# Kernel tuning notes

Hardware: AMD Instinct MI355X
Metric: run time of the kernel (lower is better)

The kernel has to match this reference:

```python
import jax, jax.numpy as jnp
import numpy as np

B, C, Q = 16, 1024, 128
XD, YD = 64, 32
D, H, HID, L = 512, 8, 2048, 6
HD = D // H
NEG = -1e9


def setup_inputs() -> dict:
    key = jax.random.key(0)
    ks = jax.random.split(key, 12)
    rn = lambda k, shape, s: jax.random.normal(k, shape, jnp.float32) * s
    return {
        "x_c": rn(ks[0], (B, C, XD), 1.0),
        "y_c": rn(ks[1], (B, C, YD), 1.0),
        "x_q": rn(ks[2], (B, Q, XD), 1.0),
        "W_val": rn(ks[3], (XD + YD, D), (XD + YD) ** -0.5),
        "b_val": jnp.zeros((D,), jnp.float32),
        "q_emb": rn(ks[4], (D,), D ** -0.5),
        "in_proj_w": rn(ks[5], (L, 3 * D, D), D ** -0.5),
        "in_proj_b": jnp.zeros((L, 3 * D), jnp.float32),
        "out_w": rn(ks[6], (L, D, D), D ** -0.5),
        "out_b": jnp.zeros((L, D), jnp.float32),
        "ln1_g": jnp.ones((L, D), jnp.float32),
        "ln1_b": jnp.zeros((L, D), jnp.float32),
        "lin1_w": rn(ks[7], (L, HID, D), D ** -0.5),
        "lin1_b": jnp.zeros((L, HID), jnp.float32),
        "lin2_w": rn(ks[8], (L, D, HID), HID ** -0.5),
        "lin2_b": jnp.zeros((L, D), jnp.float32),
        "ln2_g": jnp.ones((L, D), jnp.float32),
        "ln2_b": jnp.zeros((L, D), jnp.float32),
        "W_head": rn(ks[9], (D, YD), D ** -0.5),
        "b_head": jnp.zeros((YD,), jnp.float32),
    }


def _layernorm(x, g, b):
    mu = x.mean(-1, keepdims=True)
    var = ((x - mu) ** 2).mean(-1, keepdims=True)
    return (x - mu) * jax.lax.rsqrt(var + 1e-5) * g + b


def _forward(x_c, y_c, x_q, W_val, b_val, q_emb, in_proj_w, in_proj_b, out_w,
             out_b, ln1_g, ln1_b, lin1_w, lin1_b, lin2_w, lin2_b, ln2_g, ln2_b,
             W_head, b_head):
    bsz, c_len, _ = x_c.shape
    q_len = x_q.shape[1]
    S = c_len + q_len
    # concat y onto x; queries get zero y placeholder
    xy_c = jnp.concatenate([x_c, y_c], axis=-1)
    xy_q = jnp.concatenate([x_q, jnp.zeros((bsz, q_len, y_c.shape[-1]), x_q.dtype)], axis=-1)
    xy = jnp.concatenate([xy_c, xy_q], axis=1) @ W_val + b_val          # [B,S,D]
    xy = xy.at[:, -q_len:].add(q_emb)
    # src_mask: no one may attend to query positions (last q_len keys)
    bias = jnp.where(jnp.arange(S) >= c_len, jnp.float32(NEG), jnp.float32(0.0))  # [S] key axis

    def layer(x, p):
        ipw, ipb, ow, ob, g1, b1, w1, bb1, w2, bb2, g2, b2 = p
        qkv = x @ ipw.T + ipb                                           # [B,S,3D]
        q, k, v = jnp.split(qkv, 3, axis=-1)
        heads = lambda t: t.reshape(bsz, S, H, HD).transpose(0, 2, 1, 3)  # [B,H,S,HD]
        q, k, v = heads(q), heads(k), heads(v)
        scores = jnp.einsum('bhqd,bhkd->bhqk', q, k) / np.float32(np.sqrt(HD)) + bias
        attn = jax.nn.softmax(scores, axis=-1)
        ctx = jnp.einsum('bhqk,bhkd->bhqd', attn, v)
        ctx = ctx.transpose(0, 2, 1, 3).reshape(bsz, S, D)
        x = _layernorm(x + ctx @ ow.T + ob, g1, b1)                     # post-norm
        ff = jax.nn.relu(x @ w1.T + bb1) @ w2.T + bb2
        x = _layernorm(x + ff, g2, b2)
        return x, None

    params = (in_proj_w, in_proj_b, out_w, out_b, ln1_g, ln1_b,
              lin1_w, lin1_b, lin2_w, lin2_b, ln2_g, ln2_b)
    x, _ = jax.lax.scan(layer, xy, params)
    return x[:, -q_len:] @ W_head + b_head                              # [B,Q,YD]


def reference(x_c, y_c, x_q, W_val, b_val, q_emb, in_proj_w, in_proj_b, out_w,
              out_b, ln1_g, ln1_b, lin1_w, lin1_b, lin2_w, lin2_b, ln2_g, ln2_b,
              W_head, b_head):
    return _forward(x_c, y_c, x_q, W_val, b_val, q_emb, in_proj_w, in_proj_b,
                    out_w, out_b, ln1_g, ln1_b, lin1_w, lin1_b, lin2_w, lin2_b,
                    ln2_g, ln2_b, W_head, b_head)
```

## Files before the change

### kernel.cpp

```cpp
#include <hip/hip_runtime.h>

#define B_   16
#define C_   1024
#define Q_   128
#define S_   1152
#define D_   512
#define H_   8
#define HID_ 2048
#define L_   6
#define M_   (B_*S_)
#define MQ_  (B_*Q_)
#define QSC_ 0.18033688011f

typedef short bf16x8 __attribute__((ext_vector_type(8)));
typedef float f32x4  __attribute__((ext_vector_type(4)));
#define MFMA16(a,b,c) __builtin_amdgcn_mfma_f32_16x16x32_bf16(a,b,c,0,0,0)

__device__ __forceinline__ unsigned short f2b(float f){
  union { float f; unsigned u; } v; v.f = f;
  return (unsigned short)((v.u + 0x7FFF + ((v.u >> 16) & 1)) >> 16);
}
__device__ __forceinline__ float b2f(unsigned short u){
  return __uint_as_float((unsigned)u << 16);
}
__device__ __forceinline__ void gload16(const void* g, void* l){
  __builtin_amdgcn_global_load_lds((const __attribute__((address_space(1))) void*)g,
                                   (__attribute__((address_space(3))) void*)l, 16, 0, 0);
}
__device__ __forceinline__ float waveSum(float v){
  #pragma unroll
  for (int o = 32; o > 0; o >>= 1) v += __shfl_down(v, o, 64);
  return v;
}

__global__ __launch_bounds__(256) void f2b_kernel(
    const float* __restrict__ in, unsigned short* __restrict__ out, int n4)
{
  int i = blockIdx.x*256 + threadIdx.x;
  for (; i < n4; i += gridDim.x*256) {
    float4 v = ((const float4*)in)[i];
    ushort4 o = { f2b(v.x), f2b(v.y), f2b(v.z), f2b(v.w) };
    ((ushort4*)out)[i] = o;
  }
}

__global__ __launch_bounds__(256) void f2bq_kernel(
    const float* __restrict__ in, unsigned short* __restrict__ out, int n4)
{
  int i = blockIdx.x*256 + threadIdx.x;
  for (; i < n4; i += gridDim.x*256) {
    const int row = (i >> 7) % 1536;
    const float s = (row < 512) ? QSC_ : 1.f;
    float4 v = ((const float4*)in)[i];
    ushort4 o = { f2b(v.x*s), f2b(v.y*s), f2b(v.z*s), f2b(v.w*s) };
    ((ushort4*)out)[i] = o;
  }
}

__global__ __launch_bounds__(256) void sbias_kernel(
    const float* __restrict__ in, float* __restrict__ out)
{
  int idx = blockIdx.x*256 + threadIdx.x;
  if (idx < L_*1536) {
    int j = idx % 1536;
    out[idx] = in[idx] * (j < 512 ? QSC_ : 1.f);
  }
}

__global__ __launch_bounds__(256) void packxy_kernel(
    const float* __restrict__ x_c, const float* __restrict__ y_c,
    const float* __restrict__ x_q, unsigned short* __restrict__ XY)
{
  int idx = blockIdx.x*256 + threadIdx.x;
  const int n = M_*128;
  for (; idx < n; idx += gridDim.x*256) {
    int row = idx >> 7, col = idx & 127;
    int bb = row / S_, s = row % S_;
    float v;
    if (col < 64) {
      v = (s < C_) ? x_c[((size_t)bb*C_ + s)*64 + col]
                   : x_q[((size_t)bb*Q_ + (s - C_))*64 + col];
    } else if (col < 96) {
      v = (s < C_) ? y_c[((size_t)bb*C_ + s)*32 + (col - 64)] : 0.f;
    } else if (col == 96) {
      v = 1.f;
    } else if (col == 97) {
      v = (s >= C_) ? 1.f : 0.f;
    } else v = 0.f;
    XY[idx] = f2b(v);
  }
}

__global__ __launch_bounds__(256) void wemb_kernel(
    const float* __restrict__ W_val, const float* __restrict__ b_val,
    const float* __restrict__ q_emb, unsigned short* __restrict__ Wemb)
{
  int idx = blockIdx.x*256 + threadIdx.x;
  int nn = idx >> 7, k = idx & 127;
  float v;
  if (k < 96)       v = W_val[k*D_ + nn];
  else if (k == 96) v = b_val[nn];
  else if (k == 97) v = q_emb[nn];
  else              v = 0.f;
  Wemb[idx] = f2b(v);
}

__global__ __launch_bounds__(256) void gatherq_kernel(
    const unsigned short* __restrict__ X, unsigned short* __restrict__ Xq)
{
  int row = blockIdx.x;
  int bb = row >> 7, qi = row & 127;
  const unsigned short* src = X + ((size_t)bb*S_ + C_ + qi)*D_;
  unsigned short* dst = Xq + (size_t)row*D_;
  int tid = threadIdx.x;
  dst[tid] = src[tid];
  dst[tid + 256] = src[tid + 256];
}

#define SWZ(row) (((row) >> 1) & 3)

template<int RELU, int BOUT>
__global__ __launch_bounds__(256) void bgemm_kernel(
    const unsigned short* __restrict__ A, const unsigned short* __restrict__ W,
    const float* __restrict__ bias,
    float* __restrict__ Cf, unsigned short* __restrict__ Cb, int Nn, int Kk)
{
  __shared__ short As[2][4096];
  __shared__ short Bs[2][4096];
  int lin = blockIdx.y * gridDim.x + blockIdx.x;
  const int nwg = gridDim.x * gridDim.y;
  const int cpx = nwg >> 3;
  lin = (lin & 7) * cpx + (lin >> 3);
  const int bm = (lin / gridDim.x) * 128, bn = (lin % gridDim.x) * 128;

  const int tid = threadIdx.x;
  const int w = tid >> 6, lane = tid & 63, l15 = lane & 15, l4 = lane >> 4;
  const int wm = w >> 1, wn = w & 1;
  f32x4 acc[4][4] = {};
  const size_t strA = (size_t)Kk * 2;
  const char* Abase = (const char*)A + (size_t)bm * strA;
  const char* Wbase = (const char*)W + (size_t)bn * strA;
  const int srow = tid >> 2;
  const int schunk = (tid & 3) ^ SWZ(srow);
  const size_t soff = (size_t)srow * strA + (size_t)(schunk * 16);
  const int ldsOff = w * 1024;

#define STAGEK(K0, BUF) do { \
    const char* a0_ = Abase + soff + (size_t)(K0)*2; \
    const char* b0_ = Wbase + soff + (size_t)(K0)*2; \
    char* la_ = (char*)As + (BUF)*8192 + ldsOff; \
    char* lb_ = (char*)Bs + (BUF)*8192 + ldsOff; \
    gload16(a0_,            la_); \
    gload16(a0_ + 64*strA,  la_ + 4096); \
    gload16(b0_,            lb_); \
    gload16(b0_ + 64*strA,  lb_ + 4096); \
  } while(0)

  STAGEK(0, 0);
  const int nk = Kk >> 5;
  for (int t = 0; t < nk; t++) {
    __syncthreads();
    if (t + 1 < nk) STAGEK((t+1)*32, (t+1)&1);
    const short* AsC = (const short*)As + (t&1)*4096;
    const short* BsC = (const short*)Bs + (t&1)*4096;
    bf16x8 af[4], bfr[4];
    #pragma unroll
    for (int mf = 0; mf < 4; mf++) {
      const int ar = wm*64 + mf*16 + l15;
      af[mf] = *(const bf16x8*)(AsC + ar*32 + (l4 ^ SWZ(ar))*8);
    }
    #pragma unroll
    for (int nf = 0; nf < 4; nf++) {
      const int br = wn*64 + nf*16 + l15;
      bfr[nf] = *(const bf16x8*)(BsC + br*32 + (l4 ^ SWZ(br))*8);
    }
    #pragma unroll
    for (int mf = 0; mf < 4; mf++)
      #pragma unroll
      for (int nf = 0; nf < 4; nf++)
        acc[mf][nf] = MFMA16(af[mf], bfr[nf], acc[mf][nf]);
  }
#undef STAGEK

  #pragma unroll
  for (int mf = 0; mf < 4; mf++) {
    #pragma unroll
    for (int nf = 0; nf < 4; nf++) {
      const int ccol = bn + wn*64 + nf*16 + l15;
      const float bv = bias[ccol];
      #pragma unroll
      for (int r = 0; r < 4; r++) {
        const int rrow = bm + wm*64 + mf*16 + l4*4 + r;
        float o = acc[mf][nf][r] + bv;
        if (RELU) o = fmaxf(o, 0.f);
        if (BOUT == 1) Cb[(size_t)rrow*Nn + ccol] = f2b(o);
        else           Cf[(size_t)rrow*Nn + ccol] = o;
      }
    }
  }
}

__global__ __launch_bounds__(256) void bgemm64_kernel(
    const unsigned short* __restrict__ A, const unsigned short* __restrict__ W,
    const float* __restrict__ bias, const unsigned short* __restrict__ Rsd,
    float* __restrict__ Cf, int Nn, int Kk)
{
  __shared__ short As[2][8192];
  __shared__ short Bs[2][4096];
  int lin = blockIdx.y * gridDim.x + blockIdx.x;
  const int nwg = gridDim.x * gridDim.y;
  const int cpx = nwg >> 3;
  lin = (lin & 7) * cpx + (lin >> 3);
  const int bm = (lin / gridDim.x) * 128, bn = (lin % gridDim.x) * 64;

  const int tid = threadIdx.x;
  const int w = tid >> 6, lane = tid & 63, l15 = lane & 15, l4 = lane >> 4;
  f32x4 acc[2][4] = {};
  const size_t strA = (size_t)Kk * 2;
  const char* Abase = (const char*)A + (size_t)bm * strA;
  const char* Wbase = (const char*)W + (size_t)bn * strA;
  const int srow = tid >> 3;
  const int schunk = (tid & 7) ^ (srow & 7);
  const size_t soff = (size_t)srow * strA + (size_t)(schunk * 16);
  const int ldsOff = w * 1024;

#define STG64(K0, BUF) do { \
    const char* a0_ = Abase + soff + (size_t)(K0)*2; \
    const char* b0_ = Wbase + soff + (size_t)(K0)*2; \
    char* la_ = (char*)As + (BUF)*16384 + ldsOff; \
    char* lb_ = (char*)Bs + (BUF)*8192  + ldsOff; \
    gload16(a0_,            la_); \
    gload16(a0_ + 32*strA,  la_ + 4096); \
    gload16(a0_ + 64*strA,  la_ + 8192); \
    gload16(a0_ + 96*strA,  la_ + 12288); \
    gload16(b0_,            lb_); \
    gload16(b0_ + 32*strA,  lb_ + 4096); \
  } while(0)

  STG64(0, 0);
  const int nk = Kk >> 6;
  for (int t = 0; t < nk; t++) {
    __syncthreads();
    if (t + 1 < nk) STG64((t+1)*64, (t+1)&1);
    const short* AsC = (const short*)As + (t&1)*8192;
    const short* BsC = (const short*)Bs + (t&1)*4096;
    bf16x8 af[2][2], bfr[4][2];
    #pragma unroll
    for (int mf = 0; mf < 2; mf++) {
      const int ar = w*32 + mf*16 + l15;
      #pragma unroll
      for (int ks = 0; ks < 2; ks++) {
        const int c = ks*4 + l4;
        af[mf][ks] = *(const bf16x8*)(AsC + ar*64 + (c ^ (ar & 7))*8);
      }
    }
    #pragma unroll
    for (int nf = 0; nf < 4; nf++) {
      const int br = nf*16 + l15;
      #pragma unroll
      for (int ks = 0; ks < 2; ks++) {
        const int c = ks*4 + l4;
        bfr[nf][ks] = *(const bf16x8*)(BsC + br*64 + (c ^ (br & 7))*8);
      }
    }
    #pragma unroll
    for (int ks = 0; ks < 2; ks++)
      #pragma unroll
      for (int mf = 0; mf < 2; mf++)
        #pragma unroll
        for (int nf = 0; nf < 4; nf++)
          acc[mf][nf] = MFMA16(af[mf][ks], bfr[nf][ks], acc[mf][nf]);
  }
#undef STG64

  #pragma unroll
  for (int mf = 0; mf < 2; mf++) {
    #pragma unroll
    for (int nf = 0; nf < 4; nf++) {
      const int ccol = bn + nf*16 + l15;
      const float bv = bias[ccol];
      #pragma unroll
      for (int r = 0; r < 4; r++) {
        const int rrow = bm + w*32 + mf*16 + l4*4 + r;
        float o = acc[mf][nf][r] + bv + b2f(Rsd[(size_t)rrow*Nn + ccol]);
        Cf[(size_t)rrow*Nn + ccol] = o;
      }
    }
  }
}

__global__ __launch_bounds__(256) void mattn_kernel(
    const unsigned short* __restrict__ QKV, unsigned short* __restrict__ Ctx,
    int nqt, int qoff, int orows)
{
  __shared__ short Ks[64*72];
  __shared__ short Vt[64*72];
  __shared__ short Ps[4*16*72];
  int bid = blockIdx.x;
  const int nwg = gridDim.x;
  bid = (bid & 7) * (nwg >> 3) + (bid >> 3);
  const int qt = bid % nqt;
  const int h  = (bid / nqt) % H_;
  const int bb = bid / (nqt*H_);
  const int tid = threadIdx.x;
  const int w = tid >> 6, lane = tid & 63, l15 = lane & 15, l4 = lane >> 4;

  const size_t rowQ = (size_t)bb*S_ + qoff + (size_t)qt*64 + w*16 + l15;
  const unsigned short* qp = QKV + rowQ*1536 + h*64;
  const bf16x8 qf0 = *(const bf16x8*)(qp + l4*8);
  const bf16x8 qf1 = *(const bf16x8*)(qp + 32 + l4*8);

  const unsigned short* Kg = QKV + (size_t)bb*S_*1536 + 512 + h*64;
  const unsigned short* Vg = Kg + 512;

  f32x4 ctx[4] = {};
  f32x4 lacc = {};

  const bf16x8 onesv = {(short)0x3F80,(short)0x3F80,(short)0x3F80,(short)0x3F80,
                        (short)0x3F80,(short)0x3F80,(short)0x3F80,(short)0x3F80};

  char* PsW = (char*)Ps + w*2304;

  const int skey = tid >> 3, shc = tid & 7;
  const int vp   = tid >> 3, vhc = tid & 7;

  const unsigned short* gK = Kg + (size_t)skey*1536 + shc*8;
  const unsigned short* gV = Vg + (size_t)(2*vp)*1536 + vhc*8;
  bf16x8 k0v = *(const bf16x8*)gK;
  bf16x8 k1v = *(const bf16x8*)(gK + 32*1536);
  bf16x8 c0  = *(const bf16x8*)gV;
  bf16x8 c1  = *(const bf16x8*)(gV + 1536);

  for (int kt = 0; kt < 16; kt++) {
    __syncthreads();
    *(bf16x8*)((char*)Ks + skey*144      + shc*16) = k0v;
    *(bf16x8*)((char*)Ks + (skey+32)*144 + shc*16) = k1v;
    #pragma unroll
    for (int j = 0; j < 8; j++) {
      const int hd = vhc*8 + j;
      unsigned int val = (unsigned int)(unsigned short)c0[j]
                       | ((unsigned int)(unsigned short)c1[j] << 16);
      *(unsigned int*)((char*)Vt + hd*144 + ((4*vp) ^ (vhc<<4))) = val;
    }
    __syncthreads();
    if (kt < 15) {
      const unsigned short* nK = gK + (size_t)(kt+1)*98304;
      const unsigned short* nV = gV + (size_t)(kt+1)*98304;
      k0v = *(const bf16x8*)nK;
      k1v = *(const bf16x8*)(nK + 32*1536);
      c0  = *(const bf16x8*)nV;
      c1  = *(const bf16x8*)(nV + 1536);
    }

    f32x4 sac[4] = {};
    __builtin_amdgcn_s_setprio(1);
    #pragma unroll
    for (int nf = 0; nf < 4; nf++) {
      const char* kb = (char*)Ks + (nf*16 + l15)*144 + l4*16;
      bf16x8 b0 = *(const bf16x8*)kb;
      bf16x8 b1 = *(const bf16x8*)(kb + 64);
      sac[nf] = MFMA16(qf0, b0, sac[nf]);
      sac[nf] = MFMA16(qf1, b1, sac[nf]);
    }
    __builtin_amdgcn_s_setprio(0);

    #pragma unroll
    for (int r = 0; r < 4; r++) {
      unsigned short* pw = (unsigned short*)(PsW + (l4*4 + r)*144);
      pw[ 0 + l15] = (unsigned short)(__float_as_uint(__builtin_amdgcn_exp2f(sac[0][r])) >> 16);
      pw[16 + l15] = (unsigned short)(__float_as_uint(__builtin_amdgcn_exp2f(sac[1][r])) >> 16);
      pw[32 + l15] = (unsigned short)(__float_as_uint(__builtin_amdgcn_exp2f(sac[2][r])) >> 16);
      pw[48 + l15] = (unsigned short)(__float_as_uint(__builtin_amdgcn_exp2f(sac[3][r])) >> 16);
    }

    const char* pb = PsW + l15*144 + l4*16;
    const bf16x8 pf0 = *(const bf16x8*)pb;
    const bf16x8 pf1 = *(const bf16x8*)(pb + 64);
    __builtin_amdgcn_s_setprio(1);
    lacc = MFMA16(pf0, onesv, lacc);
    lacc = MFMA16(pf1, onesv, lacc);
    #pragma unroll
    for (int hf = 0; hf < 4; hf++) {
      const int hd = hf*16 + l15;
      const int hc = (hd >> 3) & 7;
      const char* vb = (char*)Vt + hd*144;
      bf16x8 v0 = *(const bf16x8*)(vb + ((l4*16)     ^ (hc<<4)));
      bf16x8 v1 = *(const bf16x8*)(vb + (((l4+4)*16) ^ (hc<<4)));
      ctx[hf] = MFMA16(pf0, v0, ctx[hf]);
      ctx[hf] = MFMA16(pf1, v1, ctx[hf]);
    }
    __builtin_amdgcn_s_setprio(0);
  }

  #pragma unroll
  for (int r = 0; r < 4; r++) {
    const float invl = 1.0f / lacc[r];
    const size_t row = (size_t)bb*orows + (size_t)qt*64 + w*16 + l4*4 + r;
    unsigned short* op = Ctx + row*512 + h*64;
    op[ 0 + l15] = f2b(ctx[0][r]*invl);
    op[16 + l15] = f2b(ctx[1][r]*invl);
    op[32 + l15] = f2b(ctx[2][r]*invl);
    op[48 + l15] = f2b(ctx[3][r]*invl);
  }
}

__global__ __launch_bounds__(256) void ln_kernel(
    const float* __restrict__ Yin, const float* __restrict__ g, const float* __restrict__ b,
    unsigned short* __restrict__ Xb)
{
  int row = blockIdx.x, tid = threadIdx.x;
  const float* yr = Yin + (size_t)row*D_;
  float v0 = yr[tid], v1 = yr[tid + 256];
  __shared__ float red[4];
  float s = waveSum(v0 + v1);
  if ((tid & 63) == 0) red[tid >> 6] = s;
  __syncthreads();
  float mu = (red[0] + red[1] + red[2] + red[3]) * (1.f/512.f);
  __syncthreads();
  float d0 = v0 - mu, d1 = v1 - mu;
  float ss = waveSum(d0*d0 + d1*d1);
  if ((tid & 63) == 0) red[tid >> 6] = ss;
  __syncthreads();
  float inv = rsqrtf((red[0] + red[1] + red[2] + red[3]) * (1.f/512.f) + 1e-5f);
  Xb[(size_t)row*D_ + tid]       = f2b(d0 * inv * g[tid]       + b[tid]);
  Xb[(size_t)row*D_ + tid + 256] = f2b(d1 * inv * g[tid + 256] + b[tid + 256]);
}

__global__ __launch_bounds__(64) void head_kernel(
    const unsigned short* __restrict__ Xq, const float* __restrict__ W_head,
    const float* __restrict__ b_head, float* __restrict__ out)
{
  int row = blockIdx.x;
  const unsigned short* xr = Xq + (size_t)row*D_;
  __shared__ float xs[512];
  int tid = threadIdx.x;
  for (int i = tid; i < 512; i += 64) xs[i] = b2f(xr[i]);
  __syncthreads();
  if (tid < 32) {
    float acc = b_head[tid];
    #pragma unroll 8
    for (int k = 0; k < 512; k++) acc += xs[k] * W_head[k*32 + tid];
    out[(size_t)row*32 + tid] = acc;
  }
}

extern "C" void kernel_launch(void* const* d_in, const int* in_sizes, int n_in,
                              void* d_out, int out_size, void* d_ws, size_t ws_size,
                              hipStream_t stream)
{
  const float* x_c      = (const float*)d_in[0];
  const float* y_c      = (const float*)d_in[1];
  const float* x_q      = (const float*)d_in[2];
  const float* W_val    = (const float*)d_in[3];
  const float* b_val    = (const float*)d_in[4];
  const float* q_emb    = (const float*)d_in[5];
  const float* in_proj_w= (const float*)d_in[6];
  const float* in_proj_b= (const float*)d_in[7];
  const float* out_w    = (const float*)d_in[8];
  const float* out_b    = (const float*)d_in[9];
  const float* ln1_g    = (const float*)d_in[10];
  const float* ln1_b    = (const float*)d_in[11];
  const float* lin1_w   = (const float*)d_in[12];
  const float* lin1_b   = (const float*)d_in[13];
  const float* lin2_w   = (const float*)d_in[14];
  const float* lin2_b   = (const float*)d_in[15];
  const float* ln2_g    = (const float*)d_in[16];
  const float* ln2_b    = (const float*)d_in[17];
  const float* W_head   = (const float*)d_in[18];
  const float* b_head   = (const float*)d_in[19];
  float* out = (float*)d_out;

  char* p = (char*)d_ws;
  float* Yf = (float*)p;                     p += (size_t)M_*D_*4;
  unsigned short* hid  = (unsigned short*)p; p += (size_t)M_*HID_*2;
  unsigned short* Xb2  = (unsigned short*)p; p += (size_t)M_*D_*2;
  unsigned short* qkv  = (unsigned short*)p; p += (size_t)M_*3*D_*2;
  unsigned short* Xb1  = qkv;
  unsigned short* ctxb = (unsigned short*)p; p += (size_t)M_*D_*2;
  unsigned short* ipwB = (unsigned short*)p; p += (size_t)L_*3*D_*D_*2;
  unsigned short* owB  = (unsigned short*)p; p += (size_t)L_*D_*D_*2;
  unsigned short* w1B  = (unsigned short*)p; p += (size_t)L_*HID_*D_*2;
  unsigned short* w2B  = (unsigned short*)p; p += (size_t)L_*D_*HID_*2;
  unsigned short* XYb  = (unsigned short*)p; p += (size_t)M_*128*2;
  unsigned short* Wemb = (unsigned short*)p; p += (size_t)D_*128*2;
  float* zbias         = (float*)p;          p += 2048*4;
  float* qkvbias       = (float*)p;          p += L_*1536*4;

  unsigned short* ctxq  = ctxb;
  float*          Yfq   = Yf;
  unsigned short* hidq  = hid;
  unsigned short* Xqb2  = XYb;
  unsigned short* Xqb1  = XYb + (size_t)MQ_*D_;

  (void)hipMemsetAsync(zbias, 0, 2048*4, stream);

  f2bq_kernel<<<512, 256, 0, stream>>>(in_proj_w, ipwB, L_*3*D_*D_/4);
  sbias_kernel<<<36, 256, 0, stream>>>(in_proj_b, qkvbias);
  f2b_kernel<<<512, 256, 0, stream>>>(out_w,     owB,  L_*D_*D_/4);
  f2b_kernel<<<512, 256, 0, stream>>>(lin1_w,    w1B,  L_*HID_*D_/4);
  f2b_kernel<<<512, 256, 0, stream>>>(lin2_w,    w2B,  L_*D_*HID_/4);
  wemb_kernel<<<256, 256, 0, stream>>>(W_val, b_val, q_emb, Wemb);
  packxy_kernel<<<1024, 256, 0, stream>>>(x_c, y_c, x_q, XYb);

  bgemm_kernel<0,1><<<dim3(4, 144), 256, 0, stream>>>(
      XYb, Wemb, zbias, nullptr, Xb2, D_, 128);

  for (int l = 0; l < L_ - 1; l++) {
    bgemm_kernel<0,1><<<dim3(12, 144), 256, 0, stream>>>(
        Xb2, ipwB + (size_t)l*3*D_*D_, qkvbias + (size_t)l*3*D_,
        nullptr, qkv, 3*D_, D_);
    mattn_kernel<<<B_*H_*18, 256, 0, stream>>>(qkv, ctxb, 18, 0, S_);
    bgemm64_kernel<<<dim3(8, 144), 256, 0, stream>>>(
        ctxb, owB + (size_t)l*D_*D_, out_b + (size_t)l*D_, Xb2, Yf, D_, D_);
    ln_kernel<<<M_, 256, 0, stream>>>(Yf, ln1_g + (size_t)l*D_, ln1_b + (size_t)l*D_, Xb1);
    bgemm_kernel<1,1><<<dim3(16, 144), 256, 0, stream>>>(
        Xb1, w1B + (size_t)l*HID_*D_, lin1_b + (size_t)l*HID_,
        nullptr, hid, HID_, D_);
    bgemm64_kernel<<<dim3(8, 144), 256, 0, stream>>>(
        hid, w2B + (size_t)l*D_*HID_, lin2_b + (size_t)l*D_, Xb1, Yf, D_, HID_);
    ln_kernel<<<M_, 256, 0, stream>>>(Yf, ln2_g + (size_t)l*D_, ln2_b + (size_t)l*D_, Xb2);
  }

  {
    const int l = L_ - 1;
    bgemm_kernel<0,1><<<dim3(12, 144), 256, 0, stream>>>(
        Xb2, ipwB + (size_t)l*3*D_*D_, qkvbias + (size_t)l*3*D_,
        nullptr, qkv, 3*D_, D_);
    mattn_kernel<<<B_*H_*2, 256, 0, stream>>>(qkv, ctxq, 2, C_, Q_);
    gatherq_kernel<<<MQ_, 256, 0, stream>>>(Xb2, Xqb2);
    bgemm64_kernel<<<dim3(8, 16), 256, 0, stream>>>(
        ctxq, owB + (size_t)l*D_*D_, out_b + (size_t)l*D_, Xqb2, Yfq, D_, D_);
    ln_kernel<<<MQ_, 256, 0, stream>>>(Yfq, ln1_g + (size_t)l*D_, ln1_b + (size_t)l*D_, Xqb1);
    bgemm_kernel<1,1><<<dim3(16, 16), 256, 0, stream>>>(
        Xqb1, w1B + (size_t)l*HID_*D_, lin1_b + (size_t)l*HID_,
        nullptr, hidq, HID_, D_);
    bgemm64_kernel<<<dim3(8, 16), 256, 0, stream>>>(
        hidq, w2B + (size_t)l*D_*HID_, lin2_b + (size_t)l*D_, Xqb1, Yfq, D_, HID_);
    ln_kernel<<<MQ_, 256, 0, stream>>>(Yfq, ln2_g + (size_t)l*D_, ln2_b + (size_t)l*D_, Xqb2);
  }

  head_kernel<<<MQ_, 64, 0, stream>>>(Xqb2, W_head, b_head, out);
}
```

Before: 1.585 ms.

## Double attention query tile per block and store pre-LN residual in bf16

Result: no change. 1.581 ms (-0.3%).

```diff
diff --git a/kernel.cpp b/kernel.cpp
--- a/kernel.cpp
+++ b/kernel.cpp
@@ -203,7 +203,7 @@
 __global__ __launch_bounds__(256) void bgemm64_kernel(
     const unsigned short* __restrict__ A, const unsigned short* __restrict__ W,
     const float* __restrict__ bias, const unsigned short* __restrict__ Rsd,
-    float* __restrict__ Cf, int Nn, int Kk)
+    unsigned short* __restrict__ Cb, int Nn, int Kk)
 {
   __shared__ short As[2][8192];
   __shared__ short Bs[2][4096];
@@ -283,7 +283,7 @@
       for (int r = 0; r < 4; r++) {
         const int rrow = bm + w*32 + mf*16 + l4*4 + r;
         float o = acc[mf][nf][r] + bv + b2f(Rsd[(size_t)rrow*Nn + ccol]);
-        Cf[(size_t)rrow*Nn + ccol] = o;
+        Cb[(size_t)rrow*Nn + ccol] = f2b(o);
       }
     }
   }
@@ -295,7 +295,7 @@
 {
   __shared__ short Ks[64*72];
   __shared__ short Vt[64*72];
-  __shared__ short Ps[4*16*72];
+  __shared__ short Ps[4*32*72];
   int bid = blockIdx.x;
   const int nwg = gridDim.x;
   bid = (bid & 7) * (nwg >> 3) + (bid >> 3);
@@ -305,21 +305,25 @@
   const int tid = threadIdx.x;
   const int w = tid >> 6, lane = tid & 63, l15 = lane & 15, l4 = lane >> 4;
 
-  const size_t rowQ = (size_t)bb*S_ + qoff + (size_t)qt*64 + w*16 + l15;
-  const unsigned short* qp = QKV + rowQ*1536 + h*64;
-  const bf16x8 qf0 = *(const bf16x8*)(qp + l4*8);
-  const bf16x8 qf1 = *(const bf16x8*)(qp + 32 + l4*8);
+  bf16x8 qA[2][2];
+  #pragma unroll
+  for (int g = 0; g < 2; g++) {
+    const size_t rowQ = (size_t)bb*S_ + qoff + (size_t)qt*128 + w*32 + g*16 + l15;
+    const unsigned short* qp = QKV + rowQ*1536 + h*64;
+    qA[g][0] = *(const bf16x8*)(qp + l4*8);
+    qA[g][1] = *(const bf16x8*)(qp + 32 + l4*8);
+  }
 
   const unsigned short* Kg = QKV + (size_t)bb*S_*1536 + 512 + h*64;
   const unsigned short* Vg = Kg + 512;
 
-  f32x4 ctx[4] = {};
-  f32x4 lacc = {};
+  f32x4 ctx[2][4] = {};
+  f32x4 lacc[2] = {};
 
   const bf16x8 onesv = {(short)0x3F80,(short)0x3F80,(short)0x3F80,(short)0x3F80,
                         (short)0x3F80,(short)0x3F80,(short)0x3F80,(short)0x3F80};
 
-  char* PsW = (char*)Ps + w*2304;
+  char* PsW = (char*)Ps + w*4608;
 
   const int skey = tid >> 3, shc = tid & 7;
   const int vp   = tid >> 3, vhc = tid & 7;
@@ -352,33 +356,45 @@
       c1  = *(const bf16x8*)(nV + 1536);
     }
 
-    f32x4 sac[4] = {};
+    f32x4 sac[2][4] = {};
     __builtin_amdgcn_s_setprio(1);
     #pragma unroll
     for (int nf = 0; nf < 4; nf++) {
       const char* kb = (char*)Ks + (nf*16 + l15)*144 + l4*16;
       bf16x8 b0 = *(const bf16x8*)kb;
       bf16x8 b1 = *(const bf16x8*)(kb + 64);
-      sac[nf] = MFMA16(qf0, b0, sac[nf]);
-      sac[nf] = MFMA16(qf1, b1, sac[nf]);
+      #pragma unroll
+      for (int g = 0; g < 2; g++) {
+        sac[g][nf] = MFMA16(qA[g][0], b0, sac[g][nf]);
+        sac[g][nf] = MFMA16(qA[g][1], b1, sac[g][nf]);
+      }
     }
     __builtin_amdgcn_s_setprio(0);
 
     #pragma unroll
-    for (int r = 0; r < 4; r++) {
-      unsigned short* pw = (unsigned short*)(PsW + (l4*4 + r)*144);
-      pw[ 0 + l15] = (unsigned short)(__float_as_uint(__builtin_amdgcn_exp2f(sac[0][r])) >> 16);
-      pw[16 + l15] = (unsigned short)(__float_as_uint(__builtin_amdgcn_exp2f(sac[1][r])) >> 16);
-      pw[32 + l15] = (unsigned short)(__float_as_uint(__builtin_amdgcn_exp2f(sac[2][r])) >> 16);
-      pw[48 + l15] = (unsigned short)(__float_as_uint(__builtin_amdgcn_exp2f(sac[3][r])) >> 16);
-    }
-
-    const char* pb = PsW + l15*144 + l4*16;
-    const bf16x8 pf0 = *(const bf16x8*)pb;
-    const bf16x8 pf1 = *(const bf16x8*)(pb + 64);
+    for (int g = 0; g < 2; g++)
+      #pragma unroll
+      for (int r = 0; r < 4; r++) {
+        unsigned short* pw = (unsigned short*)(PsW + (g*16 + l4*4 + r)*144);
+        pw[ 0 + l15] = (unsigned short)(__float_as_uint(__builtin_amdgcn_exp2f(sac[g][0][r])) >> 16);
+        pw[16 + l15] = (unsigned short)(__float_as_uint(__builtin_amdgcn_exp2f(sac[g][1][r])) >> 16);
+        pw[32 + l15] = (unsigned short)(__float_as_uint(__builtin_amdgcn_exp2f(sac[g][2][r])) >> 16);
+        pw[48 + l15] = (unsigned short)(__float_as_uint(__builtin_amdgcn_exp2f(sac[g][3][r])) >> 16);
+      }
+
+    bf16x8 pf[2][2];
+    #pragma unroll
+    for (int g = 0; g < 2; g++) {
+      const char* pb = PsW + (g*16 + l15)*144 + l4*16;
+      pf[g][0] = *(const bf16x8*)pb;
+      pf[g][1] = *(const bf16x8*)(pb + 64);
+    }
     __builtin_amdgcn_s_setprio(1);
-    lacc = MFMA16(pf0, onesv, lacc);
-    lacc = MFMA16(pf1, onesv, lacc);
+    #pragma unroll
+    for (int g = 0; g < 2; g++) {
+      lacc[g] = MFMA16(pf[g][0], onesv, lacc[g]);
+      lacc[g] = MFMA16(pf[g][1], onesv, lacc[g]);
+    }
     #pragma unroll
     for (int hf = 0; hf < 4; hf++) {
       const int hd = hf*16 + l15;
@@ -386,31 +402,36 @@
       const char* vb = (char*)Vt + hd*144;
       bf16x8 v0 = *(const bf16x8*)(vb + ((l4*16)     ^ (hc<<4)));
       bf16x8 v1 = *(const bf16x8*)(vb + (((l4+4)*16) ^ (hc<<4)));
-      ctx[hf] = MFMA16(pf0, v0, ctx[hf]);
-      ctx[hf] = MFMA16(pf1, v1, ctx[hf]);
+      #pragma unroll
+      for (int g = 0; g < 2; g++) {
+        ctx[g][hf] = MFMA16(pf[g][0], v0, ctx[g][hf]);
+        ctx[g][hf] = MFMA16(pf[g][1], v1, ctx[g][hf]);
+      }
     }
     __builtin_amdgcn_s_setprio(0);
   }
 
   #pragma unroll
-  for (int r = 0; r < 4; r++) {
-    const float invl = 1.0f / lacc[r];
-    const size_t row = (size_t)bb*orows + (size_t)qt*64 + w*16 + l4*4 + r;
-    unsigned short* op = Ctx + row*512 + h*64;
-    op[ 0 + l15] = f2b(ctx[0][r]*invl);
-    op[16 + l15] = f2b(ctx[1][r]*invl);
-    op[32 + l15] = f2b(ctx[2][r]*invl);
-    op[48 + l15] = f2b(ctx[3][r]*invl);
-  }
+  for (int g = 0; g < 2; g++)
+    #pragma unroll
+    for (int r = 0; r < 4; r++) {
+      const float invl = 1.0f / lacc[g][r];
+      const size_t row = (size_t)bb*orows + (size_t)qt*128 + w*32 + g*16 + l4*4 + r;
+      unsigned short* op = Ctx + row*512 + h*64;
+      op[ 0 + l15] = f2b(ctx[g][0][r]*invl);
+      op[16 + l15] = f2b(ctx[g][1][r]*invl);
+      op[32 + l15] = f2b(ctx[g][2][r]*invl);
+      op[48 + l15] = f2b(ctx[g][3][r]*invl);
+    }
 }
 
 __global__ __launch_bounds__(256) void ln_kernel(
-    const float* __restrict__ Yin, const float* __restrict__ g, const float* __restrict__ b,
+    const unsigned short* __restrict__ Yin, const float* __restrict__ g, const float* __restrict__ b,
     unsigned short* __restrict__ Xb)
 {
   int row = blockIdx.x, tid = threadIdx.x;
-  const float* yr = Yin + (size_t)row*D_;
-  float v0 = yr[tid], v1 = yr[tid + 256];
+  const unsigned short* yr = Yin + (size_t)row*D_;
+  float v0 = b2f(yr[tid]), v1 = b2f(yr[tid + 256]);
   __shared__ float red[4];
   float s = waveSum(v0 + v1);
   if ((tid & 63) == 0) red[tid >> 6] = s;
@@ -471,7 +492,7 @@
   float* out = (float*)d_out;
 
   char* p = (char*)d_ws;
-  float* Yf = (float*)p;                     p += (size_t)M_*D_*4;
+  unsigned short* Yb   = (unsigned short*)p; p += (size_t)M_*D_*2;
   unsigned short* hid  = (unsigned short*)p; p += (size_t)M_*HID_*2;
   unsigned short* Xb2  = (unsigned short*)p; p += (size_t)M_*D_*2;
   unsigned short* qkv  = (unsigned short*)p; p += (size_t)M_*3*D_*2;
@@ -487,7 +508,7 @@
   float* qkvbias       = (float*)p;          p += L_*1536*4;
 
   unsigned short* ctxq  = ctxb;
-  float*          Yfq   = Yf;
+  unsigned short* Ybq   = Yb;
   unsigned short* hidq  = hid;
   unsigned short* Xqb2  = XYb;
   unsigned short* Xqb1  = XYb + (size_t)MQ_*D_;
@@ -509,16 +530,16 @@
     bgemm_kernel<0,1><<<dim3(12, 144), 256, 0, stream>>>(
         Xb2, ipwB + (size_t)l*3*D_*D_, qkvbias + (size_t)l*3*D_,
         nullptr, qkv, 3*D_, D_);
-    mattn_kernel<<<B_*H_*18, 256, 0, stream>>>(qkv, ctxb, 18, 0, S_);
+    mattn_kernel<<<B_*H_*9, 256, 0, stream>>>(qkv, ctxb, 9, 0, S_);
     bgemm64_kernel<<<dim3(8, 144), 256, 0, stream>>>(
-        ctxb, owB + (size_t)l*D_*D_, out_b + (size_t)l*D_, Xb2, Yf, D_, D_);
-    ln_kernel<<<M_, 256, 0, stream>>>(Yf, ln1_g + (size_t)l*D_, ln1_b + (size_t)l*D_, Xb1);
+        ctxb, owB + (size_t)l*D_*D_, out_b + (size_t)l*D_, Xb2, Yb, D_, D_);
+    ln_kernel<<<M_, 256, 0, stream>>>(Yb, ln1_g + (size_t)l*D_, ln1_b + (size_t)l*D_, Xb1);
     bgemm_kernel<1,1><<<dim3(16, 144), 256, 0, stream>>>(
         Xb1, w1B + (size_t)l*HID_*D_, lin1_b + (size_t)l*HID_,
         nullptr, hid, HID_, D_);
     bgemm64_kernel<<<dim3(8, 144), 256, 0, stream>>>(
-        hid, w2B + (size_t)l*D_*HID_, lin2_b + (size_t)l*D_, Xb1, Yf, D_, HID_);
-    ln_kernel<<<M_, 256, 0, stream>>>(Yf, ln2_g + (size_t)l*D_, ln2_b + (size_t)l*D_, Xb2);
+        hid, w2B + (size_t)l*D_*HID_, lin2_b + (size_t)l*D_, Xb1, Yb, D_, HID_);
+    ln_kernel<<<M_, 256, 0, stream>>>(Yb, ln2_g + (size_t)l*D_, ln2_b + (size_t)l*D_, Xb2);
   }
 
   {
@@ -526,17 +547,17 @@
     bgemm_kernel<0,1><<<dim3(12, 144), 256, 0, stream>>>(
         Xb2, ipwB + (size_t)l*3*D_*D_, qkvbias + (size_t)l*3*D_,
         nullptr, qkv, 3*D_, D_);
-    mattn_kernel<<<B_*H_*2, 256, 0, stream>>>(qkv, ctxq, 2, C_, Q_);
+    mattn_kernel<<<B_*H_, 256, 0, stream>>>(qkv, ctxq, 1, C_, Q_);
     gatherq_kernel<<<MQ_, 256, 0, stream>>>(Xb2, Xqb2);
     bgemm64_kernel<<<dim3(8, 16), 256, 0, stream>>>(
-        ctxq, owB + (size_t)l*D_*D_, out_b + (size_t)l*D_, Xqb2, Yfq, D_, D_);
-    ln_kernel<<<MQ_, 256, 0, stream>>>(Yfq, ln1_g + (size_t)l*D_, ln1_b + (size_t)l*D_, Xqb1);
+        ctxq, owB + (size_t)l*D_*D_, out_b + (size_t)l*D_, Xqb2, Ybq, D_, D_);
+    ln_kernel<<<MQ_, 256, 0, stream>>>(Ybq, ln1_g + (size_t)l*D_, ln1_b + (size_t)l*D_, Xqb1);
     bgemm_kernel<1,1><<<dim3(16, 16), 256, 0, stream>>>(
         Xqb1, w1B + (size_t)l*HID_*D_, lin1_b + (size_t)l*HID_,
         nullptr, hidq, HID_, D_);
     bgemm64_kernel<<<dim3(8, 16), 256, 0, stream>>>(
-        hidq, w2B + (size_t)l*D_*HID_, lin2_b + (size_t)l*D_, Xqb1, Yfq, D_, HID_);
-    ln_kernel<<<MQ_, 256, 0, stream>>>(Yfq, ln2_g + (size_t)l*D_, ln2_b + (size_t)l*D_, Xqb2);
+        hidq, w2B + (size_t)l*D_*HID_, lin2_b + (size_t)l*D_, Xqb1, Ybq, D_, HID_);
+    ln_kernel<<<MQ_, 256, 0, stream>>>(Ybq, ln2_g + (size_t)l*D_, ln2_b + (size_t)l*D_, Xqb2);
   }
 
   head_kernel<<<MQ_, 64, 0, stream>>>(Xqb2, W_head, b_head, out);
```
